# Kernel optimization log

Measured on AMD Instinct MI355X. Metric: run time of the kernel, lower is better.

The kernel has to match this reference:

```python
import jax, jax.numpy as jnp
import numpy as np

N_NODES = 50000


def _scatter_softmax(alpha, row, n):
    # per-row-segment softmax over edges
    amax = jax.ops.segment_max(alpha, row, num_segments=n)
    amax = jnp.where(jnp.isfinite(amax), amax, 0.0)
    ex = jnp.exp(alpha - amax[row])
    den = jax.ops.segment_sum(ex, row, num_segments=n)
    return ex / den[row]


def setup_inputs() -> dict:
    key = jax.random.key(0)
    ks = jax.random.split(key, 10)
    N, E, H, NC, D = N_NODES, 500000, 128, 3, 3
    kv_in = H + NC * NC  # 137 (edges_in_d = 0)
    h = jax.random.normal(ks[0], (N, H), jnp.float32)
    coord = jax.random.normal(ks[1], (N, NC, D), jnp.float32)
    row = jax.random.randint(ks[2], (E,), 0, N, jnp.int32)
    col = jax.random.randint(ks[3], (E,), 0, N, jnp.int32)
    Wq = jax.random.normal(ks[4], (H, H), jnp.float32) / np.sqrt(H)
    bq = jnp.zeros((H,), jnp.float32)
    Wkv = jax.random.normal(ks[5], (kv_in, 2 * H), jnp.float32) / np.sqrt(kv_in)
    bkv = jnp.zeros((2 * H,), jnp.float32)
    Wc1 = jax.random.normal(ks[6], (H, 4 * H), jnp.float32) / np.sqrt(H)
    # torch.nn.init.xavier_uniform_(..., gain=0.001)
    Wc2 = jax.random.normal(ks[7], (4 * H, NC), jnp.float32) * 0.001
    return {"h": h, "coord": coord, "row": row, "col": col,
            "Wq": Wq, "bq": bq, "Wkv": Wkv, "bkv": bkv, "Wc1": Wc1, "Wc2": Wc2}


def reference(h, coord, row, col, Wq, bq, Wkv, bkv, Wc1, Wc2):
    N = h.shape[0]
    nc = coord.shape[1]
    # coord2radial (rm_F_norm=True: no normalization)
    coord_diff = coord[row] - coord[col]                      # [E, nc, d]
    radial = jnp.einsum('ecd,efd->ecf', coord_diff, coord_diff)  # [E, nc, nc]
    radial_flat = radial.reshape(radial.shape[0], nc * nc)
    # att_model: gather -> Q / KV linears -> interleaved k,v split
    q = h[row] @ Wq + bq                                      # [E, H]
    target_feat = jnp.concatenate([radial_flat, h[col]], axis=1)
    kv = target_feat @ Wkv + bkv                              # [E, 2H]
    k, v = kv[:, 0::2], kv[:, 1::2]
    alpha = jnp.sum(q * k, axis=1)                            # [E]
    alpha = _scatter_softmax(alpha, row, N)
    # node_model: scatter_sum aggregate (dropout is identity at eval)
    agg = jax.ops.segment_sum(alpha[:, None] * v, row, num_segments=N)
    h_out = h + agg
    # coord_model: coord_mlp(v) (MLPwoBias: linear -> SiLU -> linear, no biases)
    coord_v = alpha[:, None] * (jax.nn.silu(v @ Wc1) @ Wc2)   # [E, nc]
    trans = coord_diff * coord_v[:, :, None]                  # [E, nc, d]
    cagg = jax.ops.segment_sum(trans, row, num_segments=N)
    coord_out = coord + jnp.clip(cagg, -10.0, 10.0)
    return (h_out, coord_out, alpha)
```

## Files before the change

kernel.cpp:

```cpp
#include <hip/hip_runtime.h>

#define H 128
#define KV 256

typedef short bf16x8 __attribute__((ext_vector_type(8)));
typedef float f32x4 __attribute__((ext_vector_type(4)));
union FragU { uint4 u; bf16x8 s; };

__device__ __forceinline__ float bf2f(unsigned short u) {
  return __uint_as_float(((unsigned)u) << 16);
}
__device__ __forceinline__ unsigned short f2bf(float f) {
  unsigned b = __float_as_uint(f);
  b += 0x7FFFu + ((b >> 16) & 1u);
  return (unsigned short)(b >> 16);
}
__device__ __forceinline__ float fsilu(float x) {
  return x * __builtin_amdgcn_rcpf(1.f + __expf(-x));
}
__device__ __forceinline__ void rad6_from_cd(const float cd[9], float r6[6]) {
  r6[0] = cd[0]*cd[0] + cd[1]*cd[1] + cd[2]*cd[2];
  r6[1] = cd[3]*cd[3] + cd[4]*cd[4] + cd[5]*cd[5];
  r6[2] = cd[6]*cd[6] + cd[7]*cd[7] + cd[8]*cd[8];
  r6[3] = cd[0]*cd[3] + cd[1]*cd[4] + cd[2]*cd[5];
  r6[4] = cd[0]*cd[6] + cd[1]*cd[7] + cd[2]*cd[8];
  r6[5] = cd[3]*cd[6] + cd[4]*cd[7] + cd[5]*cd[8];
}
__constant__ int c_pa[6] = {0,4,8,1,2,5};
__constant__ int c_pb[6] = {0,0,0,3,6,7};

__global__ __launch_bounds__(256) void k_zero(float* __restrict__ p, int n) {
  int i = blockIdx.x * 256 + threadIdx.x;
  if (i < n) p[i] = 0.f;
}
__global__ __launch_bounds__(256) void k_sentinel(float* __restrict__ out, int n) {
  int i = blockIdx.x * 256 + threadIdx.x;
  if (i < n) out[i] = 1000.0f;
}

__global__ __launch_bounds__(256) void k_prep_w1(const float* __restrict__ Wc1,
                                                 uint4* __restrict__ w1f) {
  int t = blockIdx.x*256 + threadIdx.x;
  int g = t >> 6, lane = t & 63;
  int q = g >> 5, kk = (g >> 3) & 3, mt = g & 7;
  int o = q*128 + mt*16 + (lane & 15);
  int kbase = kk*32 + (lane >> 4)*8;
  unsigned s[8];
  #pragma unroll
  for (int j = 0; j < 8; ++j) s[j] = f2bf(Wc1[(kbase+j)*512 + o]);
  uint4 u;
  u.x = s[0] | (s[1]<<16); u.y = s[2] | (s[3]<<16);
  u.z = s[4] | (s[5]<<16); u.w = s[6] | (s[7]<<16);
  w1f[g*64 + lane] = u;
}

__global__ __launch_bounds__(256) void k_prep_wr6(const float* __restrict__ Wkv,
                                                  const float* __restrict__ Wc1,
                                                  float* __restrict__ Wr6) {
  int idx = blockIdx.x*256 + threadIdx.x;
  if (idx >= 6*512) return;
  int d = idx >> 9, o = idx & 511;
  float s = 0.f;
  for (int k = 0; k < 128; ++k) {
    float w = Wkv[c_pa[d]*KV + 2*k + 1];
    if (d >= 3) w += Wkv[c_pb[d]*KV + 2*k + 1];
    s += w * Wc1[k*512 + o];
  }
  Wr6[d*512 + o] = s;
}

__global__ __launch_bounds__(256) void k_prep_ar6(
    const float* __restrict__ Wr6, const float* __restrict__ Wc2,
    uint4* __restrict__ ar6f, float* __restrict__ w2p)
{
  int t = threadIdx.x;
  for (int i = t; i < 512; i += 256) {
    int ch = i;
    unsigned b0 = (unsigned)f2bf(Wr6[0*512+ch]) | ((unsigned)f2bf(Wr6[1*512+ch])<<16);
    unsigned b1 = (unsigned)f2bf(Wr6[2*512+ch]) | ((unsigned)f2bf(Wr6[3*512+ch])<<16);
    unsigned b2 = (unsigned)f2bf(Wr6[4*512+ch]) | ((unsigned)f2bf(Wr6[5*512+ch])<<16);
    ar6f[i] = make_uint4(b0, b1, b2, 0u);
  }
  for (int i = t; i < 1536; i += 256) {
    int i4 = i & 3, rest = i >> 2;
    int k = rest % 3, g = rest / 3;
    int ch = (g >> 2)*16 + (g & 3)*4 + i4;
    w2p[i] = Wc2[ch*3 + k];
  }
}

__global__ __launch_bounds__(256) void k_hist2(const int* __restrict__ row,
                                               const int* __restrict__ col,
                                               int* __restrict__ cr,
                                               int* __restrict__ cc, int E) {
  int e = blockIdx.x*256 + threadIdx.x;
  if (e >= E) return;
  atomicAdd(&cr[row[e]], 1);
  atomicAdd(&cc[col[e]], 1);
}

__global__ __launch_bounds__(1024) void k_scan2(
    const int* __restrict__ cr, int* __restrict__ rstart, int* __restrict__ rcur,
    const int* __restrict__ cc, int* __restrict__ cstart, int* __restrict__ ccur,
    int n) {
  const int* counts = (blockIdx.x == 0) ? cr : cc;
  int* start = (blockIdx.x == 0) ? rstart : cstart;
  int* cursor = (blockIdx.x == 0) ? rcur : ccur;
  __shared__ int wsum[16];
  __shared__ int carry_s;
  const int tid = threadIdx.x, lane = tid & 63, wid = tid >> 6;
  if (tid == 0) carry_s = 0;
  __syncthreads();
  for (int base = 0; base < n; base += 1024) {
    int i = base + tid;
    int v = (i < n) ? counts[i] : 0;
    int s = v;
    #pragma unroll
    for (int off = 1; off < 64; off <<= 1) {
      int t = __shfl_up(s, off, 64);
      if (lane >= off) s += t;
    }
    if (lane == 63) wsum[wid] = s;
    __syncthreads();
    if (wid == 0 && lane < 16) {
      int w = wsum[lane];
      #pragma unroll
      for (int off = 1; off < 16; off <<= 1) {
        int t = __shfl_up(w, off, 16);
        if (lane >= off) w += t;
      }
      wsum[lane] = w;
    }
    __syncthreads();
    int wexcl = (wid == 0) ? 0 : wsum[wid-1];
    int excl = carry_s + wexcl + (s - v);
    if (i < n) { start[i] = excl; cursor[i] = excl; }
    __syncthreads();
    if (tid == 0) carry_s += wsum[15];
    __syncthreads();
  }
  if (threadIdx.x == 0) start[n] = carry_s;
}

__global__ __launch_bounds__(256) void k_scatter2(
    const int* __restrict__ row, const int* __restrict__ col,
    int* __restrict__ rcur, int* __restrict__ eidx,
    int* __restrict__ ccur, int* __restrict__ eidx2, int E) {
  int e = blockIdx.x*256 + threadIdx.x;
  if (e >= E) return;
  int pos = atomicAdd(&rcur[row[e]], 1);
  eidx[pos] = e;
  int pos2 = atomicAdd(&ccur[col[e]], 1);
  eidx2[pos2] = e;
}

__global__ __launch_bounds__(384) void k_node_proj(
    const float* __restrict__ h, const float* __restrict__ Wq,
    const float* __restrict__ bq, const float* __restrict__ Wkv,
    const float* __restrict__ bkv, float* __restrict__ qn,
    float* __restrict__ kn, unsigned short* __restrict__ vn, int N)
{
  __shared__ float hs[8][H];
  const int n0 = blockIdx.x * 8;
  const int t = threadIdx.x;
  for (int idx = t; idx < 8*H; idx += 384) {
    int nn = idx >> 7, jj = idx & 127;
    hs[nn][jj] = (n0 + nn < N) ? h[(size_t)(n0+nn)*H + jj] : 0.f;
  }
  __syncthreads();
  float a[8] = {0.f,0.f,0.f,0.f,0.f,0.f,0.f,0.f};
  if (t < H) {
    #pragma unroll 4
    for (int j = 0; j < H; ++j) {
      float w = Wq[j*H + t];
      #pragma unroll
      for (int k = 0; k < 8; ++k) a[k] += hs[k][j]*w;
    }
    float b = bq[t];
    #pragma unroll
    for (int k = 0; k < 8; ++k)
      if (n0+k < N) qn[(size_t)(n0+k)*H + t] = a[k] + b;
  } else {
    int c = t - H;
    #pragma unroll 4
    for (int j = 0; j < H; ++j) {
      float w = Wkv[(9 + j)*KV + c];
      #pragma unroll
      for (int k = 0; k < 8; ++k) a[k] += hs[k][j]*w;
    }
    float b = bkv[c];
    size_t ch = (size_t)(c >> 1);
    if (c & 1) {
      #pragma unroll
      for (int k = 0; k < 8; ++k)
        if (n0+k < N) vn[(size_t)(n0+k)*H + ch] = f2bf(a[k] + b);
    } else {
      #pragma unroll
      for (int k = 0; k < 8; ++k)
        if (n0+k < N) kn[(size_t)(n0+k)*H + ch] = a[k] + b;
    }
  }
}

__global__ __launch_bounds__(256) void k_qw(
    const float* __restrict__ qn, const float* __restrict__ Wkv,
    float* __restrict__ qwn, int N)
{
  __shared__ float wke6[6*128];
  const int tid = threadIdx.x;
  for (int idx = tid; idx < 6*128; idx += 256) {
    int d = idx >> 7, j = idx & 127;
    float we = Wkv[c_pa[d]*KV + 2*j];
    if (d >= 3) we += Wkv[c_pb[d]*KV + 2*j];
    wke6[idx] = we;
  }
  __syncthreads();
  const int wid = tid >> 6, lane = tid & 63;
  const int n = blockIdx.x*4 + wid;
  if (n >= N) return;
  float q0 = qn[(size_t)n*H + lane];
  float q1 = qn[(size_t)n*H + 64 + lane];
  #pragma unroll
  for (int d = 0; d < 6; ++d) {
    float p = q0*wke6[d*128 + lane] + q1*wke6[d*128 + 64 + lane];
    #pragma unroll
    for (int m = 32; m > 0; m >>= 1) p += __shfl_xor(p, m, 64);
    if (lane == 0) qwn[(size_t)n*6 + d] = p;
  }
}

__global__ __launch_bounds__(256) void k_edge_alpha(
    const float* __restrict__ coord, const int* __restrict__ row,
    const int* __restrict__ col, const int* __restrict__ eidx,
    const float* __restrict__ qn, const float* __restrict__ kn,
    const float* __restrict__ qwn, float* __restrict__ aout, int E)
{
  int j = blockIdx.x*256 + threadIdx.x;
  if (j >= E) return;
  int e = eidx[j];
  int r = row[e], c = col[e];
  const float4* qp = (const float4*)(qn + (size_t)r*H);
  const float4* kp = (const float4*)(kn + (size_t)c*H);
  float d0 = 0.f, d1 = 0.f, d2 = 0.f, d3 = 0.f;
  #pragma unroll 8
  for (int i = 0; i < 32; ++i) {
    float4 qv = qp[i], kv = kp[i];
    d0 += qv.x*kv.x; d1 += qv.y*kv.y;
    d2 += qv.z*kv.z; d3 += qv.w*kv.w;
  }
  float cd[9], r6[6];
  #pragma unroll
  for (int i = 0; i < 9; ++i)
    cd[i] = coord[(size_t)r*9 + i] - coord[(size_t)c*9 + i];
  rad6_from_cd(cd, r6);
  float ar = (d0 + d1) + (d2 + d3);
  #pragma unroll
  for (int d = 0; d < 6; ++d) ar += r6[d]*qwn[(size_t)r*6 + d];
  aout[e] = ar;
}

__global__ __launch_bounds__(256) void k_row_soft(
    const float* __restrict__ h, const float* __restrict__ coord,
    const int* __restrict__ col, const float* __restrict__ Wkv,
    const int* __restrict__ row_start, const int* __restrict__ eidx,
    const unsigned* __restrict__ vnu, float* __restrict__ aout,
    float* __restrict__ hout, int N)
{
  __shared__ float wvo6[6*128];
  __shared__ float ws[4][64];
  __shared__ int   cs[4][64];
  const int tid = threadIdx.x;
  for (int idx = tid; idx < 6*128; idx += 256) {
    int d = idx >> 7, jj = idx & 127;
    float wo = Wkv[c_pa[d]*KV + 2*jj + 1];
    if (d >= 3) wo += Wkv[c_pb[d]*KV + 2*jj + 1];
    wvo6[idx] = wo;
  }
  __syncthreads();
  const int wid = tid >> 6, lane = tid & 63;
  const int r = blockIdx.x*4 + wid;
  if (r >= N) return;
  const int js = row_start[r], je = row_start[r+1];
  const int deg = je - js;
  float crd[9];
  #pragma unroll
  for (int i = 0; i < 9; ++i) crd[i] = coord[(size_t)r*9 + i];

  float t6s[6];
  float mn, invl;
  const bool big = (deg > 64);
  if (!big) {
    int e = 0, c = 0;
    float ar = -1e30f;
    float r6[6] = {0.f,0.f,0.f,0.f,0.f,0.f};
    if (lane < deg) {
      e = eidx[js + lane];
      ar = aout[e];
      c = col[e];
      float cd[9];
      #pragma unroll
      for (int i = 0; i < 9; ++i) cd[i] = crd[i] - coord[(size_t)c*9 + i];
      rad6_from_cd(cd, r6);
    }
    float mx = ar;
    #pragma unroll
    for (int m = 32; m > 0; m >>= 1) mx = fmaxf(mx, __shfl_xor(mx, m, 64));
    mn = mx;
    float w = (lane < deg) ? __expf(ar - mn) : 0.f;
    float lw = w;
    #pragma unroll
    for (int m = 32; m > 0; m >>= 1) lw += __shfl_xor(lw, m, 64);
    invl = (deg > 0) ? 1.f/lw : 0.f;
    #pragma unroll
    for (int d = 0; d < 6; ++d) {
      float v = w*r6[d];
      #pragma unroll
      for (int m = 32; m > 0; m >>= 1) v += __shfl_xor(v, m, 64);
      t6s[d] = v;
    }
    ws[wid][lane] = w;
    cs[wid][lane] = c;
    if (lane < deg) aout[e] = w*invl;
  } else {
    float mx = -1e30f;
    for (int j2 = js + lane; j2 < je; j2 += 64)
      mx = fmaxf(mx, aout[eidx[j2]]);
    #pragma unroll
    for (int m = 32; m > 0; m >>= 1) mx = fmaxf(mx, __shfl_xor(mx, m, 64));
    mn = mx;
    float lp = 0.f;
    float t6p[6] = {0.f,0.f,0.f,0.f,0.f,0.f};
    for (int j2 = js + lane; j2 < je; j2 += 64) {
      int e = eidx[j2];
      float ar = aout[e];
      float w = __expf(ar - mn);
      lp += w;
      int c = col[e];
      float cd[9], r6[6];
      #pragma unroll
      for (int i = 0; i < 9; ++i) cd[i] = crd[i] - coord[(size_t)c*9 + i];
      rad6_from_cd(cd, r6);
      #pragma unroll
      for (int d = 0; d < 6; ++d) t6p[d] += w*r6[d];
    }
    #pragma unroll
    for (int m = 32; m > 0; m >>= 1) lp += __shfl_xor(lp, m, 64);
    invl = (deg > 0) ? 1.f/lp : 0.f;
    #pragma unroll
    for (int d = 0; d < 6; ++d) {
      float v = t6p[d];
      #pragma unroll
      for (int m = 32; m > 0; m >>= 1) v += __shfl_xor(v, m, 64);
      t6s[d] = v;
    }
  }
  float acc0 = 0.f, acc1 = 0.f;
  if (!big) {
    #pragma unroll 4
    for (int t = 0; t < deg; ++t) {
      float w = ws[wid][t];
      int c = cs[wid][t];
      unsigned v = vnu[(size_t)c*64 + lane];
      acc0 += w*__uint_as_float(v << 16);
      acc1 += w*__uint_as_float(v & 0xffff0000u);
    }
  } else {
    for (int t = js; t < je; ++t) {
      int e = eidx[t];
      float ar = aout[e];
      float w = __expf(ar - mn);
      int c = col[e];
      unsigned v = vnu[(size_t)c*64 + lane];
      acc0 += w*__uint_as_float(v << 16);
      acc1 += w*__uint_as_float(v & 0xffff0000u);
    }
    for (int j2 = js + lane; j2 < je; j2 += 64) {
      int e = eidx[j2];
      aout[e] = __expf(aout[e] - mn)*invl;
    }
  }
  float o0 = acc0, o1 = acc1;
  #pragma unroll
  for (int d = 0; d < 6; ++d) {
    o0 += t6s[d]*wvo6[d*128 + 2*lane];
    o1 += t6s[d]*wvo6[d*128 + 2*lane + 1];
  }
  hout[(size_t)r*H + 2*lane]     = h[(size_t)r*H + 2*lane]     + o0*invl;
  hout[(size_t)r*H + 2*lane + 1] = h[(size_t)r*H + 2*lane + 1] + o1*invl;
}

__global__ __launch_bounds__(256) void k_node_hn(
    const unsigned* __restrict__ vnu, const uint4* __restrict__ w1f,
    unsigned short* __restrict__ hn, int N)
{
  __shared__ unsigned vt[128*64];
  __shared__ unsigned short hno[128*128];
  const int tid = threadIdx.x;
  const int wid = tid >> 6, lane = tid & 63;
  const int quad = lane >> 4, colc = lane & 15;
  const int n0 = blockIdx.x * 128;
  for (int i = 0; i < 32; ++i) {
    int el = i*4 + wid;
    int c = n0 + el; if (c >= N) c = N - 1;
    unsigned pk = vnu[(size_t)c*64 + lane];
    vt[el*64 + (((lane>>2) ^ (el&15))<<2) + (lane&3)] = pk;
  }
  __syncthreads();
  const int ntbase = wid*32;
  for (int q = 0; q < 4; ++q) {
    f32x4 acc[8][2];
    #pragma unroll
    for (int mt = 0; mt < 8; ++mt)
      #pragma unroll
      for (int nt = 0; nt < 2; ++nt) acc[mt][nt] = (f32x4){0.f,0.f,0.f,0.f};
    #pragma unroll
    for (int kk = 0; kk < 4; ++kk) {
      FragU bfr[2];
      #pragma unroll
      for (int nt = 0; nt < 2; ++nt) {
        int rrow = ntbase + nt*16 + colc;
        int chunk = kk*4 + quad;
        bfr[nt].u = *((const uint4*)&vt[rrow*64 + ((chunk ^ (rrow&15))<<2)]);
      }
      #pragma unroll
      for (int mt = 0; mt < 8; ++mt) {
        FragU afr;
        afr.u = w1f[(((q*4+kk)*8+mt)<<6) + lane];
        #pragma unroll
        for (int nt = 0; nt < 2; ++nt)
          acc[mt][nt] = __builtin_amdgcn_mfma_f32_16x16x32_bf16(
              afr.s, bfr[nt].s, acc[mt][nt], 0, 0, 0);
      }
    }
    #pragma unroll
    for (int mt = 0; mt < 8; ++mt)
      #pragma unroll
      for (int nt = 0; nt < 2; ++nt) {
        int node = ntbase + nt*16 + colc;
        int o = mt*16 + quad*4;
        unsigned lo = (unsigned)f2bf(acc[mt][nt][0]) | ((unsigned)f2bf(acc[mt][nt][1]) << 16);
        unsigned hi = (unsigned)f2bf(acc[mt][nt][2]) | ((unsigned)f2bf(acc[mt][nt][3]) << 16);
        *((uint2*)&hno[node*128 + o]) = make_uint2(lo, hi);
      }
    __syncthreads();
    const uint4* hns = (const uint4*)hno;
    #pragma unroll
    for (int it = 0; it < 8; ++it) {
      int u = it*256 + tid;
      int node = u >> 4, within = u & 15;
      int gn = n0 + node;
      if (gn < N) ((uint4*)hn)[(size_t)gn*64 + q*16 + within] = hns[node*16 + within];
    }
    __syncthreads();
  }
}

__global__ __launch_bounds__(256) void k_edge_mlp3(
    const float* __restrict__ coord, const int* __restrict__ row,
    const int* __restrict__ col, const uint4* __restrict__ ar6f,
    const float* __restrict__ w2p, const unsigned short* __restrict__ hn,
    const int* __restrict__ eidx2, float* __restrict__ mlpout, int E)
{
  __shared__ uint4 a8[512];
  __shared__ float4 w2s[384];
  const int tid = threadIdx.x;
  {
    const uint4* s4 = (const uint4*)w2p;
    for (int i = tid; i < 512; i += 256) a8[i] = ar6f[i];
    for (int i = tid; i < 384; i += 256) w2s[i] = ((const float4*)s4)[i];
  }
  __syncthreads();
  const int wid = tid >> 6, lane = tid & 63;
  const int l15 = lane & 15, quad = lane >> 4;
  const bool q0 = (quad == 0);

  int gw = blockIdx.x*4 + wid;
  int nw = gridDim.x*4;
  int ntile = (E + 63) >> 6;
  for (int t = gw; t < ntile; t += nw) {
    int j = t*64 + lane;
    int jc = (j < E) ? j : (E - 1);
    int e = eidx2[jc];
    int c = col[e];
    int r = row[e];
    float cd[9], r6[6];
    #pragma unroll
    for (int i = 0; i < 9; ++i)
      cd[i] = coord[(size_t)r*9 + i] - coord[(size_t)c*9 + i];
    rad6_from_cd(cd, r6);
    unsigned pw0 = (unsigned)f2bf(r6[0]) | ((unsigned)f2bf(r6[1]) << 16);
    unsigned pw1 = (unsigned)f2bf(r6[2]) | ((unsigned)f2bf(r6[3]) << 16);
    unsigned pw2 = (unsigned)f2bf(r6[4]) | ((unsigned)f2bf(r6[5]) << 16);
    FragU bfr[4];
    const unsigned short* hb[4];
    #pragma unroll
    for (int f = 0; f < 4; ++f) {
      int src = f*16 + l15;
      unsigned w0 = __shfl(pw0, src, 64);
      unsigned w1 = __shfl(pw1, src, 64);
      unsigned w2_ = __shfl(pw2, src, 64);
      bfr[f].u = make_uint4(q0 ? w0 : 0u, q0 ? w1 : 0u, q0 ? w2_ : 0u, 0u);
      int nb = __shfl(c, src, 64);
      hb[f] = hn + (size_t)nb*512 + quad*4;
    }
    float cv[4][3];
    #pragma unroll
    for (int f = 0; f < 4; ++f) { cv[f][0]=0.f; cv[f][1]=0.f; cv[f][2]=0.f; }

    const f32x4 zc = (f32x4){0.f,0.f,0.f,0.f};
    #pragma unroll 2
    for (int m = 0; m < 32; ++m) {
      uint4 av = a8[m*16 + l15];
      FragU afr;
      afr.u = make_uint4(q0 ? av.x : 0u, q0 ? av.y : 0u, q0 ? av.z : 0u, 0u);
      float4 wk0 = w2s[(m*4 + quad)*3 + 0];
      float4 wk1 = w2s[(m*4 + quad)*3 + 1];
      float4 wk2 = w2s[(m*4 + quad)*3 + 2];
      #pragma unroll
      for (int f = 0; f < 4; ++f) {
        f32x4 d = __builtin_amdgcn_mfma_f32_16x16x32_bf16(
            afr.s, bfr[f].s, zc, 0, 0, 0);
        uint2 hv = *((const uint2*)(hb[f] + m*16));
        float s0 = fsilu(d[0] + __uint_as_float(hv.x << 16));
        float s1 = fsilu(d[1] + __uint_as_float(hv.x & 0xffff0000u));
        float s2 = fsilu(d[2] + __uint_as_float(hv.y << 16));
        float s3 = fsilu(d[3] + __uint_as_float(hv.y & 0xffff0000u));
        cv[f][0] += s0*wk0.x + s1*wk0.y + s2*wk0.z + s3*wk0.w;
        cv[f][1] += s0*wk1.x + s1*wk1.y + s2*wk1.z + s3*wk1.w;
        cv[f][2] += s0*wk2.x + s1*wk2.y + s2*wk2.z + s3*wk2.w;
      }
    }
    #pragma unroll
    for (int f = 0; f < 4; ++f)
      #pragma unroll
      for (int k = 0; k < 3; ++k) {
        float v = cv[f][k];
        v += __shfl_xor(v, 16, 64);
        v += __shfl_xor(v, 32, 64);
        cv[f][k] = v;
      }
    #pragma unroll
    for (int f = 0; f < 4; ++f) {
      int src = f*16 + l15;
      int eb = __shfl(e, src, 64);
      int jb = t*64 + src;
      if (q0 && jb < E) {
        float* mp = &mlpout[(size_t)eb*3];
        mp[0] = cv[f][0]; mp[1] = cv[f][1]; mp[2] = cv[f][2];
      }
    }
  }
}

__global__ __launch_bounds__(256) void k_coord(
    const float* __restrict__ coord, const int* __restrict__ col,
    const int* __restrict__ row_start, const int* __restrict__ eidx,
    const float* __restrict__ aout, const float* __restrict__ mlpout,
    float* __restrict__ cout, int N)
{
  const int tid = threadIdx.x;
  const int wid = tid >> 6, lane = tid & 63;
  const int r = blockIdx.x*4 + wid;
  if (r >= N) return;
  const int js = row_start[r], je = row_start[r+1];
  float cr[9];
  #pragma unroll
  for (int i = 0; i < 9; ++i) cr[i] = coord[(size_t)r*9 + i];
  float cg[9] = {0.f,0.f,0.f,0.f,0.f,0.f,0.f,0.f,0.f};
  for (int j = js + lane; j < je; j += 64) {
    int e = eidx[j];
    float a = aout[e];
    int c = col[e];
    float cd[9];
    #pragma unroll
    for (int i = 0; i < 9; ++i) cd[i] = cr[i] - coord[(size_t)c*9 + i];
    float p0 = a*mlpout[(size_t)e*3+0];
    float p1 = a*mlpout[(size_t)e*3+1];
    float p2 = a*mlpout[(size_t)e*3+2];
    #pragma unroll
    for (int d = 0; d < 3; ++d) {
      cg[0+d] += p0*cd[0+d];
      cg[3+d] += p1*cd[3+d];
      cg[6+d] += p2*cd[6+d];
    }
  }
  #pragma unroll
  for (int i = 0; i < 9; ++i)
    #pragma unroll
    for (int m = 32; m > 0; m >>= 1) cg[i] += __shfl_xor(cg[i], m, 64);
  if (lane == 0) {
    #pragma unroll
    for (int i = 0; i < 9; ++i) {
      float x = fminf(10.f, fmaxf(-10.f, cg[i]));
      cout[(size_t)r*9 + i] = cr[i] + x;
    }
  }
}

extern "C" void kernel_launch(void* const* d_in, const int* in_sizes, int n_in,
                              void* d_out, int out_size, void* d_ws, size_t ws_size,
                              hipStream_t stream)
{
  const float* h     = (const float*)d_in[0];
  const float* coord = (const float*)d_in[1];
  const int* row = (const int*)d_in[2];
  const int* col = (const int*)d_in[3];
  const float* Wq  = (const float*)d_in[4];
  const float* bq  = (const float*)d_in[5];
  const float* Wkv = (const float*)d_in[6];
  const float* bkv = (const float*)d_in[7];
  const float* Wc1 = (const float*)d_in[8];
  const float* Wc2 = (const float*)d_in[9];
  const int N = in_sizes[0] / H;
  const int E = in_sizes[2];
  float* out = (float*)d_out;

  char* p = (char*)d_ws;
  float* qn = (float*)p;
  float* kn = (float*)(p + (size_t)N*H*4);
  unsigned short* hn = (unsigned short*)p;
  p += (size_t)N*H*8;
  unsigned short* vn = (unsigned short*)p;  p += (size_t)N*H*2;
  float* mlpout = (float*)p;                p += (size_t)E*3*4;
  int* counts_r = (int*)p;                  p += (size_t)N*4;
  int* counts_c = (int*)p;                  p += (size_t)N*4;
  int* row_start = (int*)p;                 p += (size_t)(N+1)*4;
  int* cursor_r = (int*)p;                  p += (size_t)N*4;
  int* cstart = (int*)p;                    p += (size_t)(N+1)*4;
  int* cursor_c = (int*)p;                  p += (size_t)N*4;
  int* eidx = (int*)p;                      p += (size_t)E*4;
  int* eidx2 = (int*)p;                     p += (size_t)E*4;
  uint4* w1f = (uint4*)((((size_t)p) + 15) & ~(size_t)15);
  float* Wr6 = (float*)((char*)w1f + 8192*16);
  uint4* ar6f = (uint4*)((char*)Wr6 + 6*512*4);
  float* w2p  = (float*)((char*)ar6f + 512*16);
  float* qwn  = (float*)((char*)w2p + 1536*4);
  const size_t need = (size_t)((char*)qwn + (size_t)N*6*4 - (char*)d_ws);

  if (ws_size < need) {
    k_sentinel<<<(out_size + 255)/256, 256, 0, stream>>>(out, out_size);
    return;
  }

  float* hout = out;
  float* cout = out + (size_t)N*H;
  float* aout = cout + (size_t)N*9;

  k_zero<<<(2*N + 255)/256, 256, 0, stream>>>((float*)counts_r, 2*N);
  k_prep_w1<<<32, 256, 0, stream>>>(Wc1, w1f);
  k_prep_wr6<<<12, 256, 0, stream>>>(Wkv, Wc1, Wr6);
  k_prep_ar6<<<1, 256, 0, stream>>>(Wr6, Wc2, ar6f, w2p);
  k_hist2<<<(E + 255)/256, 256, 0, stream>>>(row, col, counts_r, counts_c, E);
  k_node_proj<<<(N + 7)/8, 384, 0, stream>>>(h, Wq, bq, Wkv, bkv, qn, kn, vn, N);
  k_qw<<<(N + 3)/4, 256, 0, stream>>>(qn, Wkv, qwn, N);
  k_scan2<<<2, 1024, 0, stream>>>(counts_r, row_start, cursor_r,
                                  counts_c, cstart, cursor_c, N);
  k_scatter2<<<(E + 255)/256, 256, 0, stream>>>(row, col, cursor_r, eidx,
                                                cursor_c, eidx2, E);
  k_edge_alpha<<<(E + 255)/256, 256, 0, stream>>>(coord, row, col, eidx,
                                                  qn, kn, qwn, aout, E);
  k_row_soft<<<(N + 3)/4, 256, 0, stream>>>(h, coord, col, Wkv, row_start, eidx,
                                            (const unsigned*)vn, aout, hout, N);
  k_node_hn<<<(N + 127)/128, 256, 0, stream>>>((const unsigned*)vn, w1f, hn, N);
  {
    int ntile = (E + 63) >> 6;
    int blocks = (ntile + 3) >> 2;
    k_edge_mlp3<<<blocks, 256, 0, stream>>>(coord, row, col, ar6f, w2p,
                                            hn, eidx2, mlpout, E);
  }
  k_coord<<<(N + 3)/4, 256, 0, stream>>>(coord, col, row_start, eidx, aout,
                                         mlpout, cout, N);
}
```

Baseline: 755.0 us.

## Move node Q/K/V projection to split-bf16 MFMA and resize edge MLP grid

Replaces the scalar FP32 node projection kernel with an MFMA kernel. It splits both h and the weights into bf16 hi/lo parts and runs three MFMAs per tile, which keeps close to FP32 accuracy while using matrix cores. A new prep kernel packs Wq and the K/V halves of Wkv into MFMA fragment layout. Separately, the edge MLP kernel moves to 512-thread blocks with a fixed grid of 512 blocks that loops over tiles (grid-stride), replacing one launch sized to the tile count.

```diff
diff --git a/kernel.cpp b/kernel.cpp
--- a/kernel.cpp
+++ b/kernel.cpp
@@ -52,6 +52,37 @@
   u.x = s[0] | (s[1]<<16); u.y = s[2] | (s[3]<<16);
   u.z = s[4] | (s[5]<<16); u.w = s[6] | (s[7]<<16);
   w1f[g*64 + lane] = u;
+}
+
+__global__ __launch_bounds__(256) void k_prep_wcat(
+    const float* __restrict__ Wq, const float* __restrict__ Wkv,
+    uint4* __restrict__ wcat_hi, uint4* __restrict__ wcat_lo)
+{
+  int t = blockIdx.x*256 + threadIdx.x;
+  if (t >= 96*64) return;
+  int g = t >> 6, lane = t & 63;
+  int mt = g & 7, kk = (g >> 3) & 3, q = g >> 5;
+  int oo = mt*16 + (lane & 15);
+  int kbase = kk*32 + (lane >> 4)*8;
+  unsigned shi[8], slo[8];
+  #pragma unroll
+  for (int j = 0; j < 8; ++j) {
+    int k = kbase + j;
+    float w;
+    if (q == 0)      w = Wq[k*H + oo];
+    else if (q == 1) w = Wkv[(9 + k)*KV + 2*oo];
+    else             w = Wkv[(9 + k)*KV + 2*oo + 1];
+    unsigned hi = f2bf(w);
+    float lo = w - bf2f((unsigned short)hi);
+    shi[j] = hi; slo[j] = f2bf(lo);
+  }
+  uint4 uh, ul;
+  uh.x = shi[0]|(shi[1]<<16); uh.y = shi[2]|(shi[3]<<16);
+  uh.z = shi[4]|(shi[5]<<16); uh.w = shi[6]|(shi[7]<<16);
+  ul.x = slo[0]|(slo[1]<<16); ul.y = slo[2]|(slo[3]<<16);
+  ul.z = slo[4]|(slo[5]<<16); ul.w = slo[6]|(slo[7]<<16);
+  wcat_hi[g*64 + lane] = uh;
+  wcat_lo[g*64 + lane] = ul;
 }
 
 __global__ __launch_bounds__(256) void k_prep_wr6(const float* __restrict__ Wkv,
@@ -154,51 +185,93 @@
   eidx2[pos2] = e;
 }
 
-__global__ __launch_bounds__(384) void k_node_proj(
-    const float* __restrict__ h, const float* __restrict__ Wq,
-    const float* __restrict__ bq, const float* __restrict__ Wkv,
+__global__ __launch_bounds__(256) void k_node_mfma(
+    const float* __restrict__ h, const uint4* __restrict__ wcat_hi,
+    const uint4* __restrict__ wcat_lo, const float* __restrict__ bq,
     const float* __restrict__ bkv, float* __restrict__ qn,
     float* __restrict__ kn, unsigned short* __restrict__ vn, int N)
 {
-  __shared__ float hs[8][H];
-  const int n0 = blockIdx.x * 8;
-  const int t = threadIdx.x;
-  for (int idx = t; idx < 8*H; idx += 384) {
-    int nn = idx >> 7, jj = idx & 127;
-    hs[nn][jj] = (n0 + nn < N) ? h[(size_t)(n0+nn)*H + jj] : 0.f;
+  __shared__ unsigned vhi[128*64];
+  __shared__ unsigned vlo[128*64];
+  const int tid = threadIdx.x;
+  const int wid = tid >> 6, lane = tid & 63;
+  const int quad = lane >> 4, colc = lane & 15;
+  const int n0 = blockIdx.x * 128;
+  for (int i = 0; i < 32; ++i) {
+    int el = i*4 + wid;
+    int c = n0 + el; if (c >= N) c = N - 1;
+    float2 hv = *((const float2*)(h + (size_t)c*H + 2*lane));
+    unsigned h0 = f2bf(hv.x), h1 = f2bf(hv.y);
+    float l0 = hv.x - bf2f((unsigned short)h0);
+    float l1 = hv.y - bf2f((unsigned short)h1);
+    int sw = el*64 + (((lane>>2) ^ (el&15))<<2) + (lane&3);
+    vhi[sw] = h0 | (h1<<16);
+    vlo[sw] = (unsigned)f2bf(l0) | ((unsigned)f2bf(l1)<<16);
   }
   __syncthreads();
-  float a[8] = {0.f,0.f,0.f,0.f,0.f,0.f,0.f,0.f};
-  if (t < H) {
-    #pragma unroll 4
-    for (int j = 0; j < H; ++j) {
-      float w = Wq[j*H + t];
-      #pragma unroll
-      for (int k = 0; k < 8; ++k) a[k] += hs[k][j]*w;
-    }
-    float b = bq[t];
-    #pragma unroll
-    for (int k = 0; k < 8; ++k)
-      if (n0+k < N) qn[(size_t)(n0+k)*H + t] = a[k] + b;
-  } else {
-    int c = t - H;
-    #pragma unroll 4
-    for (int j = 0; j < H; ++j) {
-      float w = Wkv[(9 + j)*KV + c];
-      #pragma unroll
-      for (int k = 0; k < 8; ++k) a[k] += hs[k][j]*w;
-    }
-    float b = bkv[c];
-    size_t ch = (size_t)(c >> 1);
-    if (c & 1) {
-      #pragma unroll
-      for (int k = 0; k < 8; ++k)
-        if (n0+k < N) vn[(size_t)(n0+k)*H + ch] = f2bf(a[k] + b);
-    } else {
-      #pragma unroll
-      for (int k = 0; k < 8; ++k)
-        if (n0+k < N) kn[(size_t)(n0+k)*H + ch] = a[k] + b;
-    }
+  const int ntbase = wid*32;
+  for (int q = 0; q < 3; ++q) {
+    f32x4 acc[8][2];
+    #pragma unroll
+    for (int mt = 0; mt < 8; ++mt)
+      #pragma unroll
+      for (int nt = 0; nt < 2; ++nt) acc[mt][nt] = (f32x4){0.f,0.f,0.f,0.f};
+    #pragma unroll
+    for (int kk = 0; kk < 4; ++kk) {
+      FragU bhi[2], blo[2];
+      #pragma unroll
+      for (int nt = 0; nt < 2; ++nt) {
+        int rrow = ntbase + nt*16 + colc;
+        int ad = rrow*64 + (((kk*4 + quad) ^ (rrow&15))<<2);
+        bhi[nt].u = *((const uint4*)&vhi[ad]);
+        blo[nt].u = *((const uint4*)&vlo[ad]);
+      }
+      #pragma unroll
+      for (int mt = 0; mt < 8; ++mt) {
+        FragU ahi, alo;
+        int gidx = (((q*4+kk)*8+mt)<<6) + lane;
+        ahi.u = wcat_hi[gidx];
+        alo.u = wcat_lo[gidx];
+        #pragma unroll
+        for (int nt = 0; nt < 2; ++nt) {
+          acc[mt][nt] = __builtin_amdgcn_mfma_f32_16x16x32_bf16(
+              ahi.s, bhi[nt].s, acc[mt][nt], 0, 0, 0);
+          acc[mt][nt] = __builtin_amdgcn_mfma_f32_16x16x32_bf16(
+              ahi.s, blo[nt].s, acc[mt][nt], 0, 0, 0);
+          acc[mt][nt] = __builtin_amdgcn_mfma_f32_16x16x32_bf16(
+              alo.s, bhi[nt].s, acc[mt][nt], 0, 0, 0);
+        }
+      }
+    }
+    #pragma unroll
+    for (int mt = 0; mt < 8; ++mt)
+      #pragma unroll
+      for (int nt = 0; nt < 2; ++nt) {
+        int node = n0 + ntbase + nt*16 + colc;
+        if (node >= N) continue;
+        int chq = mt*16 + quad*4;
+        if (q == 0) {
+          float4 b = *((const float4*)(bq + chq));
+          float4 o;
+          o.x = acc[mt][nt][0] + b.x; o.y = acc[mt][nt][1] + b.y;
+          o.z = acc[mt][nt][2] + b.z; o.w = acc[mt][nt][3] + b.w;
+          *((float4*)(qn + (size_t)node*H + chq)) = o;
+        } else if (q == 1) {
+          float4 o;
+          o.x = acc[mt][nt][0] + bkv[2*(chq+0)];
+          o.y = acc[mt][nt][1] + bkv[2*(chq+1)];
+          o.z = acc[mt][nt][2] + bkv[2*(chq+2)];
+          o.w = acc[mt][nt][3] + bkv[2*(chq+3)];
+          *((float4*)(kn + (size_t)node*H + chq)) = o;
+        } else {
+          unsigned s0 = f2bf(acc[mt][nt][0] + bkv[2*(chq+0)+1]);
+          unsigned s1 = f2bf(acc[mt][nt][1] + bkv[2*(chq+1)+1]);
+          unsigned s2 = f2bf(acc[mt][nt][2] + bkv[2*(chq+2)+1]);
+          unsigned s3 = f2bf(acc[mt][nt][3] + bkv[2*(chq+3)+1]);
+          *((uint2*)(vn + (size_t)node*H + chq)) =
+              make_uint2(s0 | (s1<<16), s2 | (s3<<16));
+        }
+      }
   }
 }
 
@@ -455,7 +528,7 @@
   }
 }
 
-__global__ __launch_bounds__(256) void k_edge_mlp3(
+__global__ __launch_bounds__(512) void k_edge_mlp3(
     const float* __restrict__ coord, const int* __restrict__ row,
     const int* __restrict__ col, const uint4* __restrict__ ar6f,
     const float* __restrict__ w2p, const unsigned short* __restrict__ hn,
@@ -466,16 +539,16 @@
   const int tid = threadIdx.x;
   {
     const uint4* s4 = (const uint4*)w2p;
-    for (int i = tid; i < 512; i += 256) a8[i] = ar6f[i];
-    for (int i = tid; i < 384; i += 256) w2s[i] = ((const float4*)s4)[i];
+    for (int i = tid; i < 512; i += 512) a8[i] = ar6f[i];
+    if (tid < 384) w2s[tid] = ((const float4*)s4)[tid];
   }
   __syncthreads();
   const int wid = tid >> 6, lane = tid & 63;
   const int l15 = lane & 15, quad = lane >> 4;
   const bool q0 = (quad == 0);
 
-  int gw = blockIdx.x*4 + wid;
-  int nw = gridDim.x*4;
+  int gw = blockIdx.x*8 + wid;
+  int nw = gridDim.x*8;
   int ntile = (E + 63) >> 6;
   for (int t = gw; t < ntile; t += nw) {
     int j = t*64 + lane;
@@ -635,7 +708,9 @@
   uint4* ar6f = (uint4*)((char*)Wr6 + 6*512*4);
   float* w2p  = (float*)((char*)ar6f + 512*16);
   float* qwn  = (float*)((char*)w2p + 1536*4);
-  const size_t need = (size_t)((char*)qwn + (size_t)N*6*4 - (char*)d_ws);
+  uint4* wcat_hi = (uint4*)((char*)qwn + (size_t)N*6*4);
+  uint4* wcat_lo = (uint4*)((char*)wcat_hi + 6144*16);
+  const size_t need = (size_t)((char*)wcat_lo + 6144*16 - (char*)d_ws);
 
   if (ws_size < need) {
     k_sentinel<<<(out_size + 255)/256, 256, 0, stream>>>(out, out_size);
@@ -648,10 +723,12 @@
 
   k_zero<<<(2*N + 255)/256, 256, 0, stream>>>((float*)counts_r, 2*N);
   k_prep_w1<<<32, 256, 0, stream>>>(Wc1, w1f);
+  k_prep_wcat<<<24, 256, 0, stream>>>(Wq, Wkv, wcat_hi, wcat_lo);
   k_prep_wr6<<<12, 256, 0, stream>>>(Wkv, Wc1, Wr6);
   k_prep_ar6<<<1, 256, 0, stream>>>(Wr6, Wc2, ar6f, w2p);
   k_hist2<<<(E + 255)/256, 256, 0, stream>>>(row, col, counts_r, counts_c, E);
-  k_node_proj<<<(N + 7)/8, 384, 0, stream>>>(h, Wq, bq, Wkv, bkv, qn, kn, vn, N);
+  k_node_mfma<<<(N + 127)/128, 256, 0, stream>>>(h, wcat_hi, wcat_lo, bq, bkv,
+                                                 qn, kn, vn, N);
   k_qw<<<(N + 3)/4, 256, 0, stream>>>(qn, Wkv, qwn, N);
   k_scan2<<<2, 1024, 0, stream>>>(counts_r, row_start, cursor_r,
                                   counts_c, cstart, cursor_c, N);
@@ -662,12 +739,8 @@
   k_row_soft<<<(N + 3)/4, 256, 0, stream>>>(h, coord, col, Wkv, row_start, eidx,
                                             (const unsigned*)vn, aout, hout, N);
   k_node_hn<<<(N + 127)/128, 256, 0, stream>>>((const unsigned*)vn, w1f, hn, N);
-  {
-    int ntile = (E + 63) >> 6;
-    int blocks = (ntile + 3) >> 2;
-    k_edge_mlp3<<<blocks, 256, 0, stream>>>(coord, row, col, ar6f, w2p,
-                                            hn, eidx2, mlpout, E);
-  }
+  k_edge_mlp3<<<512, 512, 0, stream>>>(coord, row, col, ar6f, w2p,
+                                       hn, eidx2, mlpout, E);
   k_coord<<<(N + 3)/4, 256, 0, stream>>>(coord, col, row_start, eidx, aout,
                                          mlpout, cout, N);
 }
```

Result: faster. 679.4 us (-10.0%).
